# Kernel tuning notes

Measured on AMD Instinct MI355X. Metric: run time of the kernel, lower is better.

Reference implementation:

```python
import jax, jax.numpy as jnp
import numpy as np

B, S, H, NH = 1, 4096, 1024, 16
HD = H // NH  # head_dim = 64
ROPE_BASE = 10000.0


def setup_inputs() -> dict:
    key = jax.random.key(0)
    ks = jax.random.split(key, 8)
    sc = 0.02
    return {
        "hidden_states": jax.random.normal(ks[0], (B, S, H), jnp.float32),
        "attention_mask": jnp.zeros((B, 1, 1, S), jnp.float32),
        "Wq": jax.random.normal(ks[1], (H, H), jnp.float32) * sc,
        "bq": jnp.zeros((H,), jnp.float32),
        "Wk": jax.random.normal(ks[2], (H, H), jnp.float32) * sc,
        "bk": jnp.zeros((H,), jnp.float32),
        "Wv": jax.random.normal(ks[3], (H, H), jnp.float32) * sc,
        "bv": jnp.zeros((H,), jnp.float32),
    }


def _rope_tables(seq_len, head_dim, dtype):
    inv_freq = 1.0 / (ROPE_BASE ** (jnp.arange(0, head_dim, 2, dtype=jnp.float32) / head_dim))
    t = jnp.arange(seq_len, dtype=jnp.float32)
    freqs = jnp.einsum("s,d->sd", t, inv_freq)          # [S, HD/2]
    emb = jnp.concatenate([freqs, freqs], axis=-1)       # [S, HD]
    return jnp.cos(emb).astype(dtype), jnp.sin(emb).astype(dtype)


def _rotate_half(x):
    x1, x2 = jnp.split(x, 2, axis=-1)
    return jnp.concatenate([-x2, x1], axis=-1)


def reference(hidden_states, attention_mask, Wq, bq, Wk, bk, Wv, bv):
    bsz, q_len, _ = hidden_states.shape
    # QKV projections (torch Linear: x @ W.T + b), split into heads -> [B, NH, S, HD]
    def heads(x):
        return x.reshape(bsz, q_len, NH, HD).transpose(0, 2, 1, 3)
    q = heads(hidden_states @ Wq.T + bq)
    k = heads(hidden_states @ Wk.T + bk)
    v = heads(hidden_states @ Wv.T + bv)

    # RoPE with position_ids = arange(kv_seq_len)
    cos, sin = _rope_tables(q_len, HD, q.dtype)          # [S, HD]
    cos = cos[None, None]                                 # [1,1,S,HD]
    sin = sin[None, None]
    q = q * cos + _rotate_half(q) * sin
    k = k * cos + _rotate_half(k) * sin

    # Manual scaled-dot-product attention (baddbmm + softmax + matmul)
    scale = HD ** (-0.5)
    scores = jnp.einsum("bhqd,bhkd->bhqk", q, k) * scale  # [B,NH,S,S]
    scores = scores + attention_mask                      # broadcast additive mask
    weights = jax.nn.softmax(scores, axis=-1)
    attn = jnp.einsum("bhqk,bhkd->bhqd", weights, v)      # [B,NH,S,HD]

    # [B,S,NH,HD] -> [B,S,H]
    return attn.transpose(0, 2, 1, 3).reshape(bsz, q_len, NH * HD)
```

## Files before the change

### kernel.cpp

```cpp
#include <hip/hip_runtime.h>
#include <hip/hip_bf16.h>
#include <math.h>
#include <stdint.h>

#define S_ 4096
#define H_ 1024
#define NH_ 16
#define HD_ 64
#define LOG2E 1.4426950408889634f
#define QSCALE (0.125f * LOG2E)

typedef __bf16 bf16;
typedef __attribute__((ext_vector_type(8))) __bf16 bf16x8;
typedef __attribute__((ext_vector_type(4))) __bf16 bf16x4;
typedef __attribute__((ext_vector_type(4))) float f32x4;
typedef __attribute__((ext_vector_type(16))) float f32x16;
typedef __attribute__((ext_vector_type(2))) float f32x2;
typedef __attribute__((ext_vector_type(2))) int int2v;

__device__ __forceinline__ f32x4 mfma16(bf16x8 a, bf16x8 b, f32x4 c) {
    return __builtin_amdgcn_mfma_f32_16x16x32_bf16(a, b, c, 0, 0, 0);
}
__device__ __forceinline__ f32x16 mfma32(bf16x8 a, bf16x8 b, f32x16 c) {
    return __builtin_amdgcn_mfma_f32_32x32x16_bf16(a, b, c, 0, 0, 0);
}

__device__ __forceinline__ void gload16(const void* g, void* l) {
    __builtin_amdgcn_global_load_lds(
        (__attribute__((address_space(1))) void*)(uintptr_t)g,
        (__attribute__((address_space(3))) void*)(uintptr_t)l,
        16, 0, 0);
}

__device__ __forceinline__ unsigned cvtpk(float a, float b) {
    unsigned r;
    asm("v_cvt_pk_bf16_f32 %0, %1, %2" : "=v"(r) : "v"(a), "v"(b));
    return r;
}

__device__ __forceinline__ void swap32(unsigned a, unsigned b, unsigned& r0, unsigned& r1) {
#if __has_builtin(__builtin_amdgcn_permlane32_swap)
    int2v rr = __builtin_amdgcn_permlane32_swap((int)a, (int)b, false, false);
    r0 = (unsigned)rr[0];
    r1 = (unsigned)rr[1];
#else
    unsigned sa = (unsigned)__shfl_xor((int)a, 32, 64);
    unsigned sb = (unsigned)__shfl_xor((int)b, 32, 64);
    bool hi = (threadIdx.x & 32) != 0;
    r0 = hi ? sb : a;
    r1 = hi ? b : sa;
#endif
}

__device__ __forceinline__ float fexp2(float x) {
#if __has_builtin(__builtin_amdgcn_exp2f)
    return __builtin_amdgcn_exp2f(x);
#else
    return exp2f(x);
#endif
}

__global__ __launch_bounds__(256) void cvt_all_kernel(
    const float* __restrict__ hs, const float* __restrict__ Wq,
    const float* __restrict__ Wk, const float* __restrict__ Wv,
    const float* __restrict__ mask,
    bf16* __restrict__ Xb, bf16* __restrict__ Wqb,
    bf16* __restrict__ Wkb, bf16* __restrict__ Wvb,
    float2* __restrict__ tab, bf16* __restrict__ wM, float* __restrict__ wV) {
    int b = blockIdx.x;
    const float* src; bf16* dst; size_t base;
    if (b < 2048)      { src = hs; dst = Xb;  base = (size_t)b * 2048; }
    else if (b < 2560) { src = Wq; dst = Wqb; base = (size_t)(b - 2048) * 2048; }
    else if (b < 3072) { src = Wk; dst = Wkb; base = (size_t)(b - 2560) * 2048; }
    else               { src = Wv; dst = Wvb; base = (size_t)(b - 3072) * 2048; }
    size_t i = base + threadIdx.x * 8;
    float4 v0 = *reinterpret_cast<const float4*>(src + i);
    float4 v1 = *reinterpret_cast<const float4*>(src + i + 4);
    bf16x8 o;
    o[0] = (bf16)v0.x; o[1] = (bf16)v0.y; o[2] = (bf16)v0.z; o[3] = (bf16)v0.w;
    o[4] = (bf16)v1.x; o[5] = (bf16)v1.y; o[6] = (bf16)v1.z; o[7] = (bf16)v1.w;
    *reinterpret_cast<bf16x8*>(dst + i) = o;

    int idx = b * 256 + threadIdx.x;
    if (idx < S_ * 32) {
        int ii = idx & 31, s = idx >> 5;
        double ang = (double)s * exp(-(double)(2 * ii) / 64.0 * log(10000.0));
        tab[idx] = make_float2((float)cos(ang), (float)sin(ang));
    }
    if (idx < S_) {
        float e = exp2f(mask[idx] * LOG2E);
        bf16 eb = (bf16)e;
        wM[idx] = eb;
        wV[idx] = (float)eb;
    }
}

__global__ __launch_bounds__(256) void qkv_gemm_kernel(
    const bf16* __restrict__ Xb,
    const bf16* __restrict__ Wqb, const bf16* __restrict__ Wkb, const bf16* __restrict__ Wvb,
    const float* __restrict__ bqp, const float* __restrict__ bkp, const float* __restrict__ bvp,
    const float2* __restrict__ tab, const float* __restrict__ wV,
    bf16* __restrict__ Qo, bf16* __restrict__ Ko, bf16* __restrict__ Vto)
{
    __shared__ bf16 Alds[128 * 64];
    __shared__ bf16 Blds[128 * 64];
    const int z = blockIdx.z;
    const bf16* W = z == 0 ? Wqb : z == 1 ? Wkb : Wvb;
    const float* bias = z == 0 ? bqp : z == 1 ? bkp : bvp;
    const int tm = blockIdx.y * 128, tn = blockIdx.x * 128;
    const int tid = threadIdx.x, lane = tid & 63, wid = tid >> 6;
    const int wm = (wid >> 1) * 64, wn = (wid & 1) * 64;
    const int lr = lane & 15, lg = lane >> 4;
    const int c_row = tid >> 3, c_sub = tid & 7;

    f32x4 acc[4][4] = {};

    for (int kt = 0; kt < H_; kt += 64) {
        #pragma unroll
        for (int is = 0; is < 4; ++is) {
            int row = is * 32 + c_row;
            int sub = c_sub ^ (row & 7);
            gload16(&Xb[(size_t)(tm + row) * H_ + kt + sub * 8],
                    &Alds[(is * 256 + wid * 64) * 8]);
            gload16(&W[(size_t)(tn + row) * H_ + kt + sub * 8],
                    &Blds[(is * 256 + wid * 64) * 8]);
        }
        __syncthreads();

        #pragma unroll
        for (int kc = 0; kc < 2; ++kc) {
            bf16x8 af[4], bfr[4];
            #pragma unroll
            for (int mb = 0; mb < 4; ++mb) {
                int row = wm + mb * 16 + lr;
                int ch = (kc * 4 + lg) ^ (row & 7);
                af[mb] = *reinterpret_cast<const bf16x8*>(&Alds[row * 64 + ch * 8]);
            }
            #pragma unroll
            for (int nb = 0; nb < 4; ++nb) {
                int row = wn + nb * 16 + lr;
                int ch = (kc * 4 + lg) ^ (row & 7);
                bfr[nb] = *reinterpret_cast<const bf16x8*>(&Blds[row * 64 + ch * 8]);
            }
            #pragma unroll
            for (int mb = 0; mb < 4; ++mb)
                #pragma unroll
                for (int nb = 0; nb < 4; ++nb)
                    acc[mb][nb] = mfma16(af[mb], bfr[nb], acc[mb][nb]);
        }
        __syncthreads();
    }

    float bv4[4];
    #pragma unroll
    for (int nb = 0; nb < 4; ++nb) bv4[nb] = bias[tn + wn + nb * 16 + lr];

    if (z < 2) {
        bf16* Y = z == 0 ? Qo : Ko;
        const float fs = z == 0 ? QSCALE : 1.0f;
        #pragma unroll
        for (int mb = 0; mb < 4; ++mb) {
            #pragma unroll
            for (int r = 0; r < 4; ++r) {
                int row = tm + wm + mb * 16 + lg * 4 + r;
                #pragma unroll
                for (int nb = 0; nb < 2; ++nb) {
                    float2 cs = tab[row * 32 + nb * 16 + lr];
                    float x1 = acc[mb][nb][r] + bv4[nb];
                    float x2 = acc[mb][nb + 2][r] + bv4[nb + 2];
                    int col = tn + wn + nb * 16 + lr;
                    Y[(size_t)row * H_ + col]      = (bf16)((x1 * cs.x - x2 * cs.y) * fs);
                    Y[(size_t)row * H_ + col + 32] = (bf16)((x2 * cs.x + x1 * cs.y) * fs);
                }
            }
        }
    } else {
        #pragma unroll
        for (int mb = 0; mb < 4; ++mb) {
            int rowb = tm + wm + mb * 16 + lg * 4;
            float4 wv = *reinterpret_cast<const float4*>(&wV[rowb]);
            float wvr[4] = {wv.x, wv.y, wv.z, wv.w};
            #pragma unroll
            for (int nb = 0; nb < 4; ++nb) {
                int col = tn + wn + nb * 16 + lr;
                bf16x4 pk;
                #pragma unroll
                for (int r = 0; r < 4; ++r)
                    pk[r] = (bf16)((acc[mb][nb][r] + bv4[nb]) * wvr[r]);
                *reinterpret_cast<bf16x4*>(&Vto[(size_t)col * S_ + rowb]) = pk;
            }
        }
    }
}

template<int NSPLIT>
__global__ __launch_bounds__(256, 4) void attn_kernel(
    const bf16* __restrict__ Q, const bf16* __restrict__ K, const bf16* __restrict__ Vt,
    const bf16* __restrict__ wM, float* __restrict__ out,
    float* __restrict__ opart, float* __restrict__ lpart)
{
    __shared__ bf16 Kl[2][64 * 64];
    __shared__ bf16 Vl[2][64 * 64];
    const int h = blockIdx.y;
    const int qb = blockIdx.x * 128;
    const int z = blockIdx.z;
    const int tid = threadIdx.x, lane = tid & 63, wid = tid >> 6;
    const int l31 = lane & 31, hi = lane >> 5;
    const int srow = wid * 8 + (lane >> 3);
    const int ssub = (lane & 7) ^ (srow & 7);

    const int NT = S_ / 64;
    const int t0 = z * (NT / NSPLIT), t1 = t0 + NT / NSPLIT;

    bf16x8 qf[4];
    {
        const bf16* qp = &Q[(size_t)(qb + wid * 32 + l31) * H_ + h * 64 + hi * 8];
        #pragma unroll
        for (int ks = 0; ks < 4; ++ks)
            qf[ks] = *reinterpret_cast<const bf16x8*>(qp + ks * 16);
    }

    f32x16 o0 = {}, o1 = {}, lacc = {};

    const bf16* kg = &K[(size_t)(t0 * 64 + srow) * H_ + h * 64 + ssub * 8];
    const bf16* vg = &Vt[(size_t)(h * 64 + srow) * S_ + t0 * 64 + ssub * 8];

    auto STAGE = [&](int buf) {
        gload16(kg,           &Kl[buf][(wid * 8) * 64]);
        gload16(kg + 32 * H_, &Kl[buf][(32 + wid * 8) * 64]);
        gload16(vg,           &Vl[buf][(wid * 8) * 64]);
        gload16(vg + 32 * S_, &Vl[buf][(32 + wid * 8) * 64]);
        kg += 64 * H_;
        vg += 64;
    };

    STAGE(0);
    __syncthreads();
    int cur = 0;
    const bf16* wmt = wM + t0 * 64 + hi * 8;

    for (int t = t0; t < t1; ++t) {
        if (t + 1 < t1) STAGE(cur ^ 1);

        f32x16 sc0 = {}, sc1 = {};
        const bf16* Kb_ = Kl[cur];
        __builtin_amdgcn_s_setprio(1);
        #pragma unroll
        for (int ks = 0; ks < 4; ++ks) {
            int ch = (2 * ks + hi) ^ (l31 & 7);
            bf16x8 kf0 = *reinterpret_cast<const bf16x8*>(&Kb_[l31 * 64 + ch * 8]);
            sc0 = mfma32(kf0, qf[ks], sc0);
            bf16x8 kf1 = *reinterpret_cast<const bf16x8*>(&Kb_[(32 + l31) * 64 + ch * 8]);
            sc1 = mfma32(kf1, qf[ks], sc1);
        }
        __builtin_amdgcn_s_setprio(0);

        #pragma unroll
        for (int r = 0; r < 16; ++r) sc0[r] = fexp2(sc0[r]);
        #pragma unroll
        for (int r = 0; r < 16; ++r) sc1[r] = fexp2(sc1[r]);

        bf16x8 pf[4];
        #pragma unroll
        for (int ks = 0; ks < 2; ++ks) {
            unsigned w[4];
            #pragma unroll
            for (int wi = 0; wi < 2; ++wi) {
                unsigned u = cvtpk(sc0[8 * ks + 2 * wi],     sc0[8 * ks + 2 * wi + 1]);
                unsigned v = cvtpk(sc0[8 * ks + 4 + 2 * wi], sc0[8 * ks + 4 + 2 * wi + 1]);
                swap32(u, v, w[wi], w[wi + 2]);
            }
            union { unsigned u[4]; bf16x8 v; } cv;
            cv.u[0] = w[0]; cv.u[1] = w[1]; cv.u[2] = w[2]; cv.u[3] = w[3];
            pf[ks] = cv.v;
        }
        #pragma unroll
        for (int ks = 0; ks < 2; ++ks) {
            unsigned w[4];
            #pragma unroll
            for (int wi = 0; wi < 2; ++wi) {
                unsigned u = cvtpk(sc1[8 * ks + 2 * wi],     sc1[8 * ks + 2 * wi + 1]);
                unsigned v = cvtpk(sc1[8 * ks + 4 + 2 * wi], sc1[8 * ks + 4 + 2 * wi + 1]);
                swap32(u, v, w[wi], w[wi + 2]);
            }
            union { unsigned u[4]; bf16x8 v; } cv;
            cv.u[0] = w[0]; cv.u[1] = w[1]; cv.u[2] = w[2]; cv.u[3] = w[3];
            pf[2 + ks] = cv.v;
        }

        const bf16* Vb_ = Vl[cur];
        __builtin_amdgcn_s_setprio(1);
        #pragma unroll
        for (int ks = 0; ks < 4; ++ks) {
            int ch = (2 * ks + hi) ^ (l31 & 7);
            bf16x8 vf0 = *reinterpret_cast<const bf16x8*>(&Vb_[l31 * 64 + ch * 8]);
            o0 = mfma32(vf0, pf[ks], o0);
            bf16x8 vf1 = *reinterpret_cast<const bf16x8*>(&Vb_[(32 + l31) * 64 + ch * 8]);
            o1 = mfma32(vf1, pf[ks], o1);
            bf16x8 wf = *reinterpret_cast<const bf16x8*>(wmt + ks * 16);
            lacc = mfma32(wf, pf[ks], lacc);
        }
        __builtin_amdgcn_s_setprio(0);
        wmt += 64;

        __syncthreads();
        cur ^= 1;
    }

    const int q = qb + wid * 32 + l31;
    if (NSPLIT == 1) {
        float inv = 1.f / lacc[0];
        float* orow = &out[(size_t)q * H_ + h * 64];
        #pragma unroll
        for (int g2 = 0; g2 < 4; ++g2) {
            float4 a, b;
            a.x = o0[g2 * 4 + 0] * inv; a.y = o0[g2 * 4 + 1] * inv;
            a.z = o0[g2 * 4 + 2] * inv; a.w = o0[g2 * 4 + 3] * inv;
            b.x = o1[g2 * 4 + 0] * inv; b.y = o1[g2 * 4 + 1] * inv;
            b.z = o1[g2 * 4 + 2] * inv; b.w = o1[g2 * 4 + 3] * inv;
            *reinterpret_cast<float4*>(orow + 8 * g2 + 4 * hi) = a;
            *reinterpret_cast<float4*>(orow + 32 + 8 * g2 + 4 * hi) = b;
        }
    } else {
        float* op = &opart[(((size_t)z * NH_ + h) * S_ + q) * 64];
        #pragma unroll
        for (int g2 = 0; g2 < 4; ++g2) {
            float4 a, b;
            a.x = o0[g2 * 4 + 0]; a.y = o0[g2 * 4 + 1];
            a.z = o0[g2 * 4 + 2]; a.w = o0[g2 * 4 + 3];
            b.x = o1[g2 * 4 + 0]; b.y = o1[g2 * 4 + 1];
            b.z = o1[g2 * 4 + 2]; b.w = o1[g2 * 4 + 3];
            *reinterpret_cast<float4*>(op + 8 * g2 + 4 * hi) = a;
            *reinterpret_cast<float4*>(op + 32 + 8 * g2 + 4 * hi) = b;
        }
        if (hi == 0)
            lpart[((size_t)z * NH_ + h) * S_ + q] = lacc[0];
    }
}

__global__ __launch_bounds__(256) void combine_kernel(const float* __restrict__ opart,
                                                      const float* __restrict__ lpart,
                                                      float* __restrict__ out) {
    int idx = blockIdx.x * 256 + threadIdx.x;
    int d4 = idx & 15;
    int q = (idx >> 4) & 4095;
    int h = idx >> 16;
    float l0 = lpart[(size_t)h * S_ + q];
    float l1 = lpart[((size_t)NH_ + h) * S_ + q];
    float inv = 1.f / (l0 + l1);
    float4 a = *reinterpret_cast<const float4*>(&opart[(((size_t)h) * S_ + q) * 64 + d4 * 4]);
    float4 b = *reinterpret_cast<const float4*>(&opart[(((size_t)NH_ + h) * S_ + q) * 64 + d4 * 4]);
    float4 r;
    r.x = (a.x + b.x) * inv;
    r.y = (a.y + b.y) * inv;
    r.z = (a.z + b.z) * inv;
    r.w = (a.w + b.w) * inv;
    *reinterpret_cast<float4*>(&out[(size_t)q * H_ + h * 64 + d4 * 4]) = r;
}

extern "C" void kernel_launch(void* const* d_in, const int* in_sizes, int n_in,
                              void* d_out, int out_size, void* d_ws, size_t ws_size,
                              hipStream_t stream) {
    const float* hs   = (const float*)d_in[0];
    const float* mask = (const float*)d_in[1];
    const float* Wq   = (const float*)d_in[2];
    const float* bq   = (const float*)d_in[3];
    const float* Wk   = (const float*)d_in[4];
    const float* bk   = (const float*)d_in[5];
    const float* Wv   = (const float*)d_in[6];
    const float* bv   = (const float*)d_in[7];
    float* out = (float*)d_out;

    char* ws = (char*)d_ws;
    bf16* Xb    = (bf16*)(ws);
    bf16* Wqb   = (bf16*)(ws + (8u  << 20));
    bf16* Wkb   = (bf16*)(ws + (10u << 20));
    bf16* Wvb   = (bf16*)(ws + (12u << 20));
    bf16* Qb    = (bf16*)(ws + (14u << 20));
    bf16* Kb    = (bf16*)(ws + (22u << 20));
    bf16* Vt    = (bf16*)(ws + (30u << 20));
    float2* tab = (float2*)(ws + (38u << 20));
    bf16* wM    = (bf16*)(ws + (39u << 20));
    float* wV   = (float*)(ws + (39u << 20) + 65536);
    float* opart = (float*)(ws + (40u << 20));
    float* lpart = (float*)(ws + (72u << 20));
    const size_t NEED = (size_t)73u << 20;

    cvt_all_kernel<<<3584, 256, 0, stream>>>(hs, Wq, Wk, Wv, mask,
                                             Xb, Wqb, Wkb, Wvb, tab, wM, wV);
    qkv_gemm_kernel<<<dim3(H_ / 128, S_ / 128, 3), 256, 0, stream>>>(
        Xb, Wqb, Wkb, Wvb, bq, bk, bv, tab, wV, Qb, Kb, Vt);

    if (ws_size >= NEED) {
        attn_kernel<2><<<dim3(S_ / 128, NH_, 2), 256, 0, stream>>>(
            Qb, Kb, Vt, wM, out, opart, lpart);
        combine_kernel<<<(S_ * NH_ * 16) / 256, 256, 0, stream>>>(opart, lpart, out);
    } else {
        attn_kernel<1><<<dim3(S_ / 128, NH_, 1), 256, 0, stream>>>(
            Qb, Kb, Vt, wM, out, nullptr, nullptr);
    }
}
```

Measured before the change: 155.5 us.

## Fuse split-K combine into attention via atomic counter and remap blocks per XCD

Removes the separate combine kernel. The second of each pair of split blocks now merges its partial output with the other's through an atomic counter and a threadfence, then writes the normalized result. The grid becomes 1D with a swizzle that maps block indices across the 8 XCDs, so blocks sharing a head and split land on the same XCD for K/V cache reuse. This saves one launch and one full re-read of every partial, at the cost of atomics, fences and an extra counter reset in the convert kernel.

Measured after the change: 343.4 us. +120.9%, slower.

```diff
diff --git a/kernel.cpp b/kernel.cpp
--- a/kernel.cpp
+++ b/kernel.cpp
@@ -66,7 +66,8 @@
     const float* __restrict__ mask,
     bf16* __restrict__ Xb, bf16* __restrict__ Wqb,
     bf16* __restrict__ Wkb, bf16* __restrict__ Wvb,
-    float2* __restrict__ tab, bf16* __restrict__ wM, float* __restrict__ wV) {
+    float2* __restrict__ tab, bf16* __restrict__ wM, float* __restrict__ wV,
+    int* __restrict__ cnt) {
     int b = blockIdx.x;
     const float* src; bf16* dst; size_t base;
     if (b < 2048)      { src = hs; dst = Xb;  base = (size_t)b * 2048; }
@@ -93,6 +94,7 @@
         wM[idx] = eb;
         wV[idx] = (float)eb;
     }
+    if (idx < NH_ * 32) cnt[idx] = 0;
 }
 
 __global__ __launch_bounds__(256) void qkv_gemm_kernel(
@@ -197,13 +199,25 @@
 __global__ __launch_bounds__(256, 4) void attn_kernel(
     const bf16* __restrict__ Q, const bf16* __restrict__ K, const bf16* __restrict__ Vt,
     const bf16* __restrict__ wM, float* __restrict__ out,
-    float* __restrict__ opart, float* __restrict__ lpart)
+    float* __restrict__ opart, float* __restrict__ lpart, int* __restrict__ cnt)
 {
     __shared__ bf16 Kl[2][64 * 64];
     __shared__ bf16 Vl[2][64 * 64];
-    const int h = blockIdx.y;
-    const int qb = blockIdx.x * 128;
-    const int z = blockIdx.z;
+    __shared__ int finsh;
+    int x, h, z;
+    if (NSPLIT == 2) {
+        int lin = blockIdx.x;
+        int xcd = lin & 7, j = lin >> 3;
+        int pair = xcd + 8 * (j >> 5);
+        x = j & 31;
+        h = pair & 15;
+        z = pair >> 4;
+    } else {
+        x = blockIdx.x & 31;
+        h = blockIdx.x >> 5;
+        z = 0;
+    }
+    const int qb = x * 128;
     const int tid = threadIdx.x, lane = tid & 63, wid = tid >> 6;
     const int l31 = lane & 31, hi = lane >> 5;
     const int srow = wid * 8 + (lane >> 3);
@@ -335,27 +349,33 @@
         }
         if (hi == 0)
             lpart[((size_t)z * NH_ + h) * S_ + q] = lacc[0];
-    }
-}
-
-__global__ __launch_bounds__(256) void combine_kernel(const float* __restrict__ opart,
-                                                      const float* __restrict__ lpart,
-                                                      float* __restrict__ out) {
-    int idx = blockIdx.x * 256 + threadIdx.x;
-    int d4 = idx & 15;
-    int q = (idx >> 4) & 4095;
-    int h = idx >> 16;
-    float l0 = lpart[(size_t)h * S_ + q];
-    float l1 = lpart[((size_t)NH_ + h) * S_ + q];
-    float inv = 1.f / (l0 + l1);
-    float4 a = *reinterpret_cast<const float4*>(&opart[(((size_t)h) * S_ + q) * 64 + d4 * 4]);
-    float4 b = *reinterpret_cast<const float4*>(&opart[(((size_t)NH_ + h) * S_ + q) * 64 + d4 * 4]);
-    float4 r;
-    r.x = (a.x + b.x) * inv;
-    r.y = (a.y + b.y) * inv;
-    r.z = (a.z + b.z) * inv;
-    r.w = (a.w + b.w) * inv;
-    *reinterpret_cast<float4*>(&out[(size_t)q * H_ + h * 64 + d4 * 4]) = r;
+
+        __threadfence();
+        __syncthreads();
+        if (tid == 0)
+            finsh = atomicAdd(&cnt[h * 32 + x], 1);
+        __syncthreads();
+        if (finsh == 1) {
+            __threadfence();
+            const int zo = 1 - z;
+            const float* opo = &opart[(((size_t)zo * NH_ + h) * S_ + q) * 64];
+            float lo_ = lpart[((size_t)zo * NH_ + h) * S_ + q];
+            float inv = 1.f / (lacc[0] + lo_);
+            float* orow = &out[(size_t)q * H_ + h * 64];
+            #pragma unroll
+            for (int g2 = 0; g2 < 4; ++g2) {
+                float4 ao = *reinterpret_cast<const float4*>(opo + 8 * g2 + 4 * hi);
+                float4 bo = *reinterpret_cast<const float4*>(opo + 32 + 8 * g2 + 4 * hi);
+                float4 a, b;
+                a.x = (o0[g2 * 4 + 0] + ao.x) * inv; a.y = (o0[g2 * 4 + 1] + ao.y) * inv;
+                a.z = (o0[g2 * 4 + 2] + ao.z) * inv; a.w = (o0[g2 * 4 + 3] + ao.w) * inv;
+                b.x = (o1[g2 * 4 + 0] + bo.x) * inv; b.y = (o1[g2 * 4 + 1] + bo.y) * inv;
+                b.z = (o1[g2 * 4 + 2] + bo.z) * inv; b.w = (o1[g2 * 4 + 3] + bo.w) * inv;
+                *reinterpret_cast<float4*>(orow + 8 * g2 + 4 * hi) = a;
+                *reinterpret_cast<float4*>(orow + 32 + 8 * g2 + 4 * hi) = b;
+            }
+        }
+    }
 }
 
 extern "C" void kernel_launch(void* const* d_in, const int* in_sizes, int n_in,
@@ -384,19 +404,19 @@
     float* wV   = (float*)(ws + (39u << 20) + 65536);
     float* opart = (float*)(ws + (40u << 20));
     float* lpart = (float*)(ws + (72u << 20));
+    int*   cnt   = (int*)(ws + (72u << 20) + (512u << 10));
     const size_t NEED = (size_t)73u << 20;
 
     cvt_all_kernel<<<3584, 256, 0, stream>>>(hs, Wq, Wk, Wv, mask,
-                                             Xb, Wqb, Wkb, Wvb, tab, wM, wV);
+                                             Xb, Wqb, Wkb, Wvb, tab, wM, wV, cnt);
     qkv_gemm_kernel<<<dim3(H_ / 128, S_ / 128, 3), 256, 0, stream>>>(
         Xb, Wqb, Wkb, Wvb, bq, bk, bv, tab, wV, Qb, Kb, Vt);
 
     if (ws_size >= NEED) {
-        attn_kernel<2><<<dim3(S_ / 128, NH_, 2), 256, 0, stream>>>(
-            Qb, Kb, Vt, wM, out, opart, lpart);
-        combine_kernel<<<(S_ * NH_ * 16) / 256, 256, 0, stream>>>(opart, lpart, out);
+        attn_kernel<2><<<1024, 256, 0, stream>>>(
+            Qb, Kb, Vt, wM, out, opart, lpart, cnt);
     } else {
-        attn_kernel<1><<<dim3(S_ / 128, NH_, 1), 256, 0, stream>>>(
-            Qb, Kb, Vt, wM, out, nullptr, nullptr);
-    }
-}
+        attn_kernel<1><<<512, 256, 0, stream>>>(
+            Qb, Kb, Vt, wM, out, nullptr, nullptr, nullptr);
+    }
+}
```
